# Optimization experiments

Hardware: AMD Instinct MI355X
Metric: run time of the kernel (lower is better)

## Reference

```python
import jax, jax.numpy as jnp
import numpy as np
import math

B, T, D, H = 8, 1024, 512, 8
DK = D // H


def setup_inputs() -> dict:
    key = jax.random.key(0)
    ks = jax.random.split(key, 16)
    f = lambda k, s: jax.random.normal(k, s, dtype=jnp.float32)
    p = lambda k, s: jax.random.normal(k, s, dtype=jnp.float32) * 0.02
    return {
        "query": f(ks[0], (B, T, D)),
        "key": f(ks[1], (B, T, D)),
        "value": f(ks[2], (B, T, D)),
        "pos_embedding": f(ks[3], (B, T, D)),
        "Wq": p(ks[4], (D, D)), "bq": p(ks[5], (D,)),
        "Wk": p(ks[6], (D, D)), "bk": p(ks[7], (D,)),
        "Wv": p(ks[8], (D, D)), "bv": p(ks[9], (D,)),
        "Wp": p(ks[10], (D, D)),
        "u_bias": p(ks[11], (H, DK)),
        "v_bias": p(ks[12], (H, DK)),
        "Wo": p(ks[13], (D, D)), "bo": p(ks[14], (D,)),
    }


def _rel_shift(pos_score):
    # pos_score: [B, H, T, T]  -> Transformer-XL relative shift via pad/reshape
    b, h, t1, t2 = pos_score.shape
    padded = jnp.concatenate(
        [jnp.zeros((b, h, t1, 1), pos_score.dtype), pos_score], axis=-1
    )  # [B,H,T,T+1]
    padded = padded.reshape(b, h, t2 + 1, t1)
    return padded[:, :, 1:].reshape(b, h, t1, t2)


def reference(query, key, value, pos_embedding, Wq, bq, Wk, bk, Wv, bv, Wp,
              u_bias, v_bias, Wo, bo):
    q = (query @ Wq + bq).reshape(B, T, H, DK)          # [B,T,H,DK]
    k = (key @ Wk + bk).reshape(B, T, H, DK)
    v = (value @ Wv + bv).reshape(B, T, H, DK)
    p = (pos_embedding @ Wp).reshape(B, T, H, DK)

    content_score = jnp.einsum("bihd,bjhd->bhij", q + u_bias, k)
    pos_score = jnp.einsum("bihd,bjhd->bhij", q + v_bias, p)
    pos_score = _rel_shift(pos_score)

    score = (content_score + pos_score) / math.sqrt(D)  # note: sqrt(d_model)
    attn = jax.nn.softmax(score, axis=-1)               # dropout: eval mode
    context = jnp.einsum("bhij,bjhd->bihd", attn, v).reshape(B, T, D)
    return context @ Wo + bo
```

## Files before the change

kernel.cpp:

```cpp
#include <hip/hip_runtime.h>

#define B_ 8
#define T_ 1024
#define D_ 512
#define H_ 8
#define DK_ 64

typedef __bf16 bf16x8 __attribute__((ext_vector_type(8)));
typedef float f32x4 __attribute__((ext_vector_type(4)));

#define MFMA16(a, b, c) __builtin_amdgcn_mfma_f32_16x16x32_bf16(a, b, c, 0, 0, 0)

__device__ __forceinline__ bf16x8 pack8(float4 a, float4 b) {
  bf16x8 r;
  r[0] = (__bf16)a.x; r[1] = (__bf16)a.y; r[2] = (__bf16)a.z; r[3] = (__bf16)a.w;
  r[4] = (__bf16)b.x; r[5] = (__bf16)b.y; r[6] = (__bf16)b.z; r[7] = (__bf16)b.w;
  return r;
}

__device__ __forceinline__ void load_lds16(const void* g, void* l) {
  __builtin_amdgcn_global_load_lds(
      (const __attribute__((address_space(1))) void*)g,
      (__attribute__((address_space(3))) void*)l, 16, 0, 0);
}

__global__ __launch_bounds__(256) void cvt_x(const float* __restrict__ q,
                                             const float* __restrict__ k,
                                             const float* __restrict__ v,
                                             const float* __restrict__ p,
                                             __bf16* __restrict__ dst) {
  const float* src = (blockIdx.y == 0) ? q
                   : (blockIdx.y == 1) ? k
                   : (blockIdx.y == 2) ? v : p;
  const size_t e = ((size_t)blockIdx.x * 256 + threadIdx.x) * 8;
  const int row = (int)(e >> 9);
  const int kk = (int)(e & 511);
  const int phys = (kk & ~63) | ((((kk >> 3) & 7) ^ (row & 7)) << 3);
  float4 a = *(const float4*)(src + e);
  float4 b = *(const float4*)(src + e + 4);
  *(bf16x8*)(dst + (size_t)blockIdx.y * 4194304 + (size_t)row * 512 + phys) =
      pack8(a, b);
}

__global__ __launch_bounds__(256) void cvt_w(const float* __restrict__ w0,
                                             const float* __restrict__ w1,
                                             const float* __restrict__ w2,
                                             const float* __restrict__ w3,
                                             const float* __restrict__ w4,
                                             __bf16* __restrict__ wt) {
  __shared__ float Ts[64][65];
  const float* W = (blockIdx.z == 0) ? w0
                 : (blockIdx.z == 1) ? w1
                 : (blockIdx.z == 2) ? w2
                 : (blockIdx.z == 3) ? w3 : w4;
  const int tid = threadIdx.x;
  const int kt = blockIdx.x * 64, nt = blockIdx.y * 64;
  const int r = tid >> 2, co = (tid & 3) * 16;
#pragma unroll
  for (int q = 0; q < 4; ++q)
    *(float4*)&Ts[r][co + q * 4] =
        *(const float4*)(W + (size_t)(kt + r) * 512 + nt + co + q * 4);
  __syncthreads();
  bf16x8 o0, o1;
#pragma unroll
  for (int q = 0; q < 8; ++q) o0[q] = (__bf16)Ts[co + q][r];
#pragma unroll
  for (int q = 0; q < 8; ++q) o1[q] = (__bf16)Ts[co + 8 + q][r];
  const int key = r & 7;
  __bf16* dst =
      wt + (size_t)blockIdx.z * 262144 + (size_t)(nt + r) * 512 + kt;
  *(bf16x8*)(dst + (((co >> 3) ^ key) << 3)) = o0;
  *(bf16x8*)(dst + ((((co >> 3) + 1) ^ key) << 3)) = o1;
}

template <int PHASE>
__global__ __launch_bounds__(256, 4) void gemm_dma(
    const __bf16* __restrict__ Xc, const __bf16* __restrict__ ctxA,
    const __bf16* __restrict__ Wt, const float* __restrict__ bq,
    const float* __restrict__ bk, const float* __restrict__ bv,
    const float* __restrict__ bo, const float* __restrict__ u,
    const float* __restrict__ v, __bf16* __restrict__ quB,
    __bf16* __restrict__ qvB, __bf16* __restrict__ kB,
    __bf16* __restrict__ vT, __bf16* __restrict__ pB,
    float* __restrict__ out) {
  __shared__ __bf16 smem[17408];
  __bf16* As = smem;
  __bf16* Bs = smem + 8192;
  const int tid = threadIdx.x;
  const int z = blockIdx.z;
  const int wave = tid >> 6, lane = tid & 63, l16 = lane & 15, quad = lane >> 4;
  const int wm = wave & 1, wn = wave >> 1;
  const int m0 = blockIdx.x * 128, n0 = blockIdx.y * 128;

  const __bf16* Ag = PHASE ? ctxA : Xc + (size_t)z * (8192 * 512);
  const __bf16* Bg = Wt + (size_t)(PHASE ? 4 : z) * (512 * 512);

  const int drow = tid >> 3, dch = (tid & 7) * 8;
  char* ldsA = (char*)As + (tid & 192) * 16;
  char* ldsB = (char*)Bs + (tid & 192) * 16;
  const int keyc = l16 & 7;

  f32x4 acc[4][4];
#pragma unroll
  for (int rb = 0; rb < 4; ++rb)
#pragma unroll
    for (int cb = 0; cb < 4; ++cb) acc[rb][cb] = 0.f;

#pragma unroll 1
  for (int k0 = 0; k0 < 512; k0 += 64) {
    __syncthreads();
#pragma unroll
    for (int c4 = 0; c4 < 4; ++c4) {
      load_lds16(Ag + (size_t)(m0 + c4 * 32 + drow) * 512 + k0 + dch,
                 ldsA + c4 * 4096);
      load_lds16(Bg + (size_t)(n0 + c4 * 32 + drow) * 512 + k0 + dch,
                 ldsB + c4 * 4096);
    }
    __syncthreads();
#pragma unroll
    for (int s = 0; s < 2; ++s) {
      const int ph = ((s * 4 + quad) ^ keyc) << 3;
      bf16x8 afr[4], bfr[4];
#pragma unroll
      for (int rb = 0; rb < 4; ++rb)
        afr[rb] = *(const bf16x8*)&As[(wm * 64 + rb * 16 + l16) * 64 + ph];
#pragma unroll
      for (int cb = 0; cb < 4; ++cb)
        bfr[cb] = *(const bf16x8*)&Bs[(wn * 64 + cb * 16 + l16) * 64 + ph];
#pragma unroll
      for (int rb = 0; rb < 4; ++rb)
#pragma unroll
        for (int cb = 0; cb < 4; ++cb)
          acc[rb][cb] = MFMA16(afr[rb], bfr[cb], acc[rb][cb]);
    }
  }

  if (PHASE == 1) {
#pragma unroll
    for (int rb = 0; rb < 4; ++rb)
#pragma unroll
      for (int cb = 0; cb < 4; ++cb) {
        const int col = n0 + wn * 64 + cb * 16 + l16;
        const float bb = bo[col];
#pragma unroll
        for (int r = 0; r < 4; ++r) {
          const int row = m0 + wm * 64 + rb * 16 + quad * 4 + r;
          out[(size_t)row * 512 + col] = acc[rb][cb][r] + bb;
        }
      }
    return;
  }

  if (z == 2) {
    __syncthreads();
    __bf16* Tt = smem;
#pragma unroll
    for (int rb = 0; rb < 4; ++rb)
#pragma unroll
      for (int cb = 0; cb < 4; ++cb) {
        const int cl = wn * 64 + cb * 16 + l16;
        const float bb = bv[n0 + cl];
#pragma unroll
        for (int r = 0; r < 4; ++r) {
          const int rl = wm * 64 + rb * 16 + quad * 4 + r;
          Tt[cl * 136 + rl] = (__bf16)(acc[rb][cb][r] + bb);
        }
      }
    __syncthreads();
    const int r2 = tid >> 1, ch = (tid & 1) * 64;
    const int hh = (n0 + r2) >> 6, dkk = (n0 + r2) & 63;
    const int bI = m0 >> 10, t0 = m0 & 1023;
    __bf16* dst = vT + (((size_t)(bI * H_ + hh)) * DK_ + dkk) * T_ + t0 + ch;
#pragma unroll
    for (int q = 0; q < 8; ++q)
      *(bf16x8*)(dst + q * 8) = *(const bf16x8*)&Tt[r2 * 136 + ch + q * 8];
    return;
  }

#pragma unroll
  for (int rb = 0; rb < 4; ++rb)
#pragma unroll
    for (int cb = 0; cb < 4; ++cb) {
      const int col = n0 + wn * 64 + cb * 16 + l16;
      const float bb = (z == 0) ? bq[col] : (z == 1) ? bk[col] : 0.f;
      const float uu = (z == 0) ? u[col] : 0.f;
      const float vv = (z == 0) ? v[col] : 0.f;
#pragma unroll
      for (int r = 0; r < 4; ++r) {
        const int row = m0 + wm * 64 + rb * 16 + quad * 4 + r;
        const float val = acc[rb][cb][r] + bb;
        const int bI = row >> 10, tt = row & 1023;
        const int hh = col >> 6, dk = col & 63;
        const size_t idx = (((size_t)(bI * H_ + hh)) * T_ + tt) * DK_ + dk;
        if (z == 0) {
          quB[idx] = (__bf16)(val + uu);
          qvB[idx] = (__bf16)(val + vv);
        } else if (z == 1) {
          kB[idx] = (__bf16)val;
        } else {
          pB[idx] = (__bf16)val;
        }
      }
    }
}

__global__ __launch_bounds__(256, 3) void attn_mfma(
    const __bf16* __restrict__ qu, const __bf16* __restrict__ qv,
    const __bf16* __restrict__ kbuf, const __bf16* __restrict__ vT,
    const __bf16* __restrict__ pbuf, __bf16* __restrict__ ctx) {
  constexpr float SCALE = 0.044194173824159216f;
  __shared__ __bf16 Kt[64 * 72];
  __shared__ __bf16 Vt[64 * 72];
  __shared__ __bf16 Pb[128 * 72];
  __shared__ __bf16 Rs[66 * 68];

  const int tid = threadIdx.x;
  const int wave = tid >> 6, lane = tid & 63, l16 = lane & 15, quad = lane >> 4;
  const int g = blockIdx.x;
  const int bhq = (g & 7) * 8 + (g >> 7);
  const int i0 = ((g >> 3) & 15) * 64;
  const size_t bh = (size_t)bhq * T_ * DK_;
  const __bf16* QU = qu + bh;
  const __bf16* QV = qv + bh;
  const __bf16* Kg = kbuf + bh;
  const __bf16* Vg = vT + bh;
  const __bf16* Pg = pbuf + bh;

  bf16x8 quA[2], qvw[2], qv4[2];
  {
    const int rw = i0 + wave * 16 + l16;
    const int r4g = i0 + 64 + l16;
    const int r4 = (r4g < T_) ? r4g : T_ - 1;
#pragma unroll
    for (int s = 0; s < 2; ++s) {
      const int ko = s * 32 + quad * 8;
      quA[s] = *(const bf16x8*)&QU[(size_t)rw * DK_ + ko];
      qvw[s] = *(const bf16x8*)&QV[(size_t)rw * DK_ + ko];
      qv4[s] = *(const bf16x8*)&QV[(size_t)r4 * DK_ + ko];
    }
  }

  f32x4 Oacc[4];
#pragma unroll
  for (int cb = 0; cb < 4; ++cb) Oacc[cb] = 0.f;
  float lrun[4];
#pragma unroll
  for (int r = 0; r < 4; ++r) lrun[r] = 0.f;

  const int rbase = wave * 16 + quad * 4;
  const int kr = tid >> 2, kko = (tid & 3) * 16;
  const int vd = tid >> 2, vjo = (tid & 3) * 16;
  const int po = tid >> 1, pko = (tid & 1) * 32;

  bf16x8 kpre[2], vpre[2], ppre[4];
#define LOAD_KVP(JT)                                                          \
  {                                                                           \
    const int j0_ = (JT) * 64;                                                \
    const __bf16* ks_ = Kg + (size_t)(j0_ + kr) * DK_ + kko;                  \
    kpre[0] = *(const bf16x8*)ks_;                                            \
    kpre[1] = *(const bf16x8*)(ks_ + 8);                                      \
    const __bf16* vs_ = Vg + (size_t)vd * T_ + j0_ + vjo;                     \
    vpre[0] = *(const bf16x8*)vs_;                                            \
    vpre[1] = *(const bf16x8*)(vs_ + 8);                                      \
    int cs_ = T_ - 65 + j0_ - i0;                                             \
    if (cs_ < 0) cs_ += T_;                                                   \
    if (cs_ >= T_) cs_ -= T_;                                                 \
    int prow_ = cs_ + po;                                                     \
    if (prow_ >= T_) prow_ -= T_;                                             \
    const __bf16* ps_ = Pg + (size_t)prow_ * DK_ + pko;                       \
    ppre[0] = *(const bf16x8*)ps_;                                            \
    ppre[1] = *(const bf16x8*)(ps_ + 8);                                      \
    ppre[2] = *(const bf16x8*)(ps_ + 16);                                     \
    ppre[3] = *(const bf16x8*)(ps_ + 24);                                     \
  }

  LOAD_KVP(0)

#pragma unroll 1
  for (int jt = 0; jt < 16; ++jt) {
    const int j0 = jt * 64;
    __syncthreads();
    *(bf16x8*)&Kt[kr * 72 + kko] = kpre[0];
    *(bf16x8*)&Kt[kr * 72 + kko + 8] = kpre[1];
    *(bf16x8*)&Vt[vd * 72 + vjo] = vpre[0];
    *(bf16x8*)&Vt[vd * 72 + vjo + 8] = vpre[1];
    *(bf16x8*)&Pb[po * 72 + pko] = ppre[0];
    *(bf16x8*)&Pb[po * 72 + pko + 8] = ppre[1];
    *(bf16x8*)&Pb[po * 72 + pko + 16] = ppre[2];
    *(bf16x8*)&Pb[po * 72 + pko + 24] = ppre[3];
    __syncthreads();
    if (jt < 15) LOAD_KVP(jt + 1)

    f32x4 sA[4];
#pragma unroll
    for (int cb = 0; cb < 4; ++cb) sA[cb] = 0.f;
#pragma unroll
    for (int s = 0; s < 2; ++s)
#pragma unroll
      for (int cb = 0; cb < 4; ++cb) {
        bf16x8 kf = *(const bf16x8*)&Kt[(cb * 16 + l16) * 72 + s * 32 + quad * 8];
        sA[cb] = MFMA16(quA[s], kf, sA[cb]);
      }

#pragma unroll
    for (int c = 0; c < 5; ++c) {
      const int cb = 3 - wave + c;
      f32x4 rc = 0.f;
#pragma unroll
      for (int s = 0; s < 2; ++s) {
        bf16x8 pf = *(const bf16x8*)&Pb[(cb * 16 + l16) * 72 + s * 32 + quad * 8];
        rc = MFMA16(qvw[s], pf, rc);
      }
      const int col = cb * 16 + l16;
#pragma unroll
      for (int rr = 0; rr < 4; ++rr) {
        const int dj = col + rbase + rr - 64;
        if (dj >= 0 && dj < 64) Rs[(rbase + rr) * 68 + dj] = (__bf16)rc[rr];
      }
    }
    {
      const int cb = wave;
      f32x4 rc = 0.f;
#pragma unroll
      for (int s = 0; s < 2; ++s) {
        bf16x8 pf = *(const bf16x8*)&Pb[(cb * 16 + l16) * 72 + s * 32 + quad * 8];
        rc = MFMA16(qv4[s], pf, rc);
      }
      if (quad == 0) Rs[64 * 68 + cb * 16 + l16] = (__bf16)rc[0];
    }
    __syncthreads();

    __bf16* Pa = Pb;
#pragma unroll
    for (int r = 0; r < 4; ++r) {
#pragma unroll
      for (int cb = 0; cb < 4; ++cb) {
        const int di = rbase + r;
        const int dj = cb * 16 + l16;
        const int ji = (j0 + dj) - (i0 + di);
        float pos = 0.f;
        if (ji != 1) pos = (float)Rs[(di + (ji >= 2 ? 1 : 0)) * 68 + dj];
        const float w_ = __expf((sA[cb][r] + pos) * SCALE);
        lrun[r] += w_;
        Pa[di * 68 + dj] = (__bf16)w_;
      }
    }

#pragma unroll
    for (int s = 0; s < 2; ++s) {
      bf16x8 ap = *(const bf16x8*)&Pa[(wave * 16 + l16) * 68 + s * 32 + quad * 8];
#pragma unroll
      for (int cb = 0; cb < 4; ++cb) {
        bf16x8 bv = *(const bf16x8*)&Vt[(cb * 16 + l16) * 72 + s * 32 + quad * 8];
        Oacc[cb] = MFMA16(ap, bv, Oacc[cb]);
      }
    }
  }

  float inv[4];
#pragma unroll
  for (int r = 0; r < 4; ++r) {
    float L = lrun[r];
    L += __shfl_xor(L, 1);
    L += __shfl_xor(L, 2);
    L += __shfl_xor(L, 4);
    L += __shfl_xor(L, 8);
    inv[r] = 1.f / L;
  }
  const int b = bhq >> 3, h = bhq & 7;
#pragma unroll
  for (int cb = 0; cb < 4; ++cb)
#pragma unroll
    for (int r = 0; r < 4; ++r) {
      const int row = i0 + rbase + r;
      const int chunk = cb * 2 + (l16 >> 3);
      const int col = h * DK_ + ((chunk ^ (row & 7)) << 3) + (l16 & 7);
      ctx[((size_t)(b * T_ + row)) * D_ + col] = (__bf16)(Oacc[cb][r] * inv[r]);
    }
}

extern "C" void kernel_launch(void* const* d_in, const int* in_sizes, int n_in,
                              void* d_out, int out_size, void* d_ws,
                              size_t ws_size, hipStream_t stream) {
  const float* query = (const float*)d_in[0];
  const float* key   = (const float*)d_in[1];
  const float* value = (const float*)d_in[2];
  const float* pos   = (const float*)d_in[3];
  const float* Wq = (const float*)d_in[4];
  const float* bq = (const float*)d_in[5];
  const float* Wk = (const float*)d_in[6];
  const float* bk = (const float*)d_in[7];
  const float* Wv = (const float*)d_in[8];
  const float* bv = (const float*)d_in[9];
  const float* Wp = (const float*)d_in[10];
  const float* ub = (const float*)d_in[11];
  const float* vbias = (const float*)d_in[12];
  const float* Wo = (const float*)d_in[13];
  const float* bo = (const float*)d_in[14];
  float* out = (float*)d_out;

  char* ws = (char*)d_ws;
  const size_t ACT = (size_t)8192 * 512 * 2;
  __bf16* Xc  = (__bf16*)ws;
  __bf16* quB = (__bf16*)(ws + 4 * ACT);
  __bf16* qvB = (__bf16*)(ws + 5 * ACT);
  __bf16* kB  = (__bf16*)(ws + 6 * ACT);
  __bf16* pB  = (__bf16*)(ws + 7 * ACT);
  __bf16* vT  = (__bf16*)(ws + 8 * ACT);
  __bf16* Wt  = (__bf16*)(ws + 9 * ACT);
  __bf16* ctx = Xc;

  cvt_x<<<dim3(2048, 4), 256, 0, stream>>>(query, key, value, pos, Xc);
  cvt_w<<<dim3(8, 8, 5), 256, 0, stream>>>(Wq, Wk, Wv, Wp, Wo, Wt);

  gemm_dma<0><<<dim3(64, 4, 4), 256, 0, stream>>>(
      Xc, nullptr, Wt, bq, bk, bv, bo, ub, vbias, quB, qvB, kB, vT, pB,
      nullptr);

  attn_mfma<<<dim3(1024), 256, 0, stream>>>(quB, qvB, kB, vT, pB, ctx);

  gemm_dma<1><<<dim3(64, 4, 1), 256, 0, stream>>>(
      nullptr, ctx, Wt, bq, bk, bv, bo, ub, vbias, quB, qvB, kB, vT, pB,
      out);
}
```

Before: 292.1 us.

## Load positional fragments directly from global into registers, shrink LDS, raise occupancy

The positional-embedding tile is no longer staged through shared memory. Each wave now loads its MFMA B-fragments straight from global memory into registers at the top of each iteration. This shrinks LDS to a dedicated 64x68 probability buffer and raises the launch-bounds occupancy hint from 3 to 4 blocks. The trade-off is that the P loads are no longer prefetched one iteration ahead, so their latency is exposed before the barrier. Rows overlapping between waves are also fetched redundantly from global/L2, and register pressure under the tighter launch bound may cause spills.

```diff
diff --git a/kernel.cpp b/kernel.cpp
--- a/kernel.cpp
+++ b/kernel.cpp
@@ -204,14 +204,14 @@
     }
 }
 
-__global__ __launch_bounds__(256, 3) void attn_mfma(
+__global__ __launch_bounds__(256, 4) void attn_mfma(
     const __bf16* __restrict__ qu, const __bf16* __restrict__ qv,
     const __bf16* __restrict__ kbuf, const __bf16* __restrict__ vT,
     const __bf16* __restrict__ pbuf, __bf16* __restrict__ ctx) {
   constexpr float SCALE = 0.044194173824159216f;
   __shared__ __bf16 Kt[64 * 72];
   __shared__ __bf16 Vt[64 * 72];
-  __shared__ __bf16 Pb[128 * 72];
+  __shared__ __bf16 Pa[64 * 68];
   __shared__ __bf16 Rs[66 * 68];
 
   const int tid = threadIdx.x;
@@ -250,10 +250,9 @@
   const int rbase = wave * 16 + quad * 4;
   const int kr = tid >> 2, kko = (tid & 3) * 16;
   const int vd = tid >> 2, vjo = (tid & 3) * 16;
-  const int po = tid >> 1, pko = (tid & 1) * 32;
-
-  bf16x8 kpre[2], vpre[2], ppre[4];
-#define LOAD_KVP(JT)                                                          \
+
+  bf16x8 kpre[2], vpre[2];
+#define LOAD_KV(JT)                                                           \
   {                                                                           \
     const int j0_ = (JT) * 64;                                                \
     const __bf16* ks_ = Kg + (size_t)(j0_ + kr) * DK_ + kko;                  \
@@ -262,34 +261,42 @@
     const __bf16* vs_ = Vg + (size_t)vd * T_ + j0_ + vjo;                     \
     vpre[0] = *(const bf16x8*)vs_;                                            \
     vpre[1] = *(const bf16x8*)(vs_ + 8);                                      \
-    int cs_ = T_ - 65 + j0_ - i0;                                             \
-    if (cs_ < 0) cs_ += T_;                                                   \
-    if (cs_ >= T_) cs_ -= T_;                                                 \
-    int prow_ = cs_ + po;                                                     \
-    if (prow_ >= T_) prow_ -= T_;                                             \
-    const __bf16* ps_ = Pg + (size_t)prow_ * DK_ + pko;                       \
-    ppre[0] = *(const bf16x8*)ps_;                                            \
-    ppre[1] = *(const bf16x8*)(ps_ + 8);                                      \
-    ppre[2] = *(const bf16x8*)(ps_ + 16);                                     \
-    ppre[3] = *(const bf16x8*)(ps_ + 24);                                     \
-  }
-
-  LOAD_KVP(0)
+  }
+
+  LOAD_KV(0)
 
 #pragma unroll 1
   for (int jt = 0; jt < 16; ++jt) {
     const int j0 = jt * 64;
+
+    int cs = T_ - 65 + j0 - i0;
+    if (cs < 0) cs += T_;
+    if (cs >= T_) cs -= T_;
+    bf16x8 pf[5][2], pfx[2];
+#pragma unroll
+    for (int c = 0; c < 5; ++c) {
+      const int brow = (3 - wave + c) * 16 + l16;
+      int prow = cs + brow;
+      if (prow >= T_) prow -= T_;
+      const __bf16* ps = Pg + (size_t)prow * DK_ + quad * 8;
+      pf[c][0] = *(const bf16x8*)ps;
+      pf[c][1] = *(const bf16x8*)(ps + 32);
+    }
+    {
+      int prow = cs + wave * 16 + l16;
+      if (prow >= T_) prow -= T_;
+      const __bf16* ps = Pg + (size_t)prow * DK_ + quad * 8;
+      pfx[0] = *(const bf16x8*)ps;
+      pfx[1] = *(const bf16x8*)(ps + 32);
+    }
+
     __syncthreads();
     *(bf16x8*)&Kt[kr * 72 + kko] = kpre[0];
     *(bf16x8*)&Kt[kr * 72 + kko + 8] = kpre[1];
     *(bf16x8*)&Vt[vd * 72 + vjo] = vpre[0];
     *(bf16x8*)&Vt[vd * 72 + vjo + 8] = vpre[1];
-    *(bf16x8*)&Pb[po * 72 + pko] = ppre[0];
-    *(bf16x8*)&Pb[po * 72 + pko + 8] = ppre[1];
-    *(bf16x8*)&Pb[po * 72 + pko + 16] = ppre[2];
-    *(bf16x8*)&Pb[po * 72 + pko + 24] = ppre[3];
-    __syncthreads();
-    if (jt < 15) LOAD_KVP(jt + 1)
+    __syncthreads();
+    if (jt < 15) LOAD_KV(jt + 1)
 
     f32x4 sA[4];
 #pragma unroll
@@ -307,10 +314,7 @@
       const int cb = 3 - wave + c;
       f32x4 rc = 0.f;
 #pragma unroll
-      for (int s = 0; s < 2; ++s) {
-        bf16x8 pf = *(const bf16x8*)&Pb[(cb * 16 + l16) * 72 + s * 32 + quad * 8];
-        rc = MFMA16(qvw[s], pf, rc);
-      }
+      for (int s = 0; s < 2; ++s) rc = MFMA16(qvw[s], pf[c][s], rc);
       const int col = cb * 16 + l16;
 #pragma unroll
       for (int rr = 0; rr < 4; ++rr) {
@@ -319,18 +323,13 @@
       }
     }
     {
-      const int cb = wave;
       f32x4 rc = 0.f;
 #pragma unroll
-      for (int s = 0; s < 2; ++s) {
-        bf16x8 pf = *(const bf16x8*)&Pb[(cb * 16 + l16) * 72 + s * 32 + quad * 8];
-        rc = MFMA16(qv4[s], pf, rc);
-      }
-      if (quad == 0) Rs[64 * 68 + cb * 16 + l16] = (__bf16)rc[0];
-    }
-    __syncthreads();
-
-    __bf16* Pa = Pb;
+      for (int s = 0; s < 2; ++s) rc = MFMA16(qv4[s], pfx[s], rc);
+      if (quad == 0) Rs[64 * 68 + wave * 16 + l16] = (__bf16)rc[0];
+    }
+    __syncthreads();
+
 #pragma unroll
     for (int r = 0; r < 4; ++r) {
 #pragma unroll
```

New measurement: 486.7 us. 1.67x slower.
